# Performance work log

Measured on AMD Instinct MI355X. Metric: run time of the kernel, lower is better.

The kernel has to match this reference:

```python
import jax, jax.numpy as jnp
import numpy as np

B, S, L, D = 16, 24, 128, 768
A, T = 8, 8
VOCAB = 100


def setup_inputs() -> dict:
    key = jax.random.key(0)
    k1, k2, k3, k4, k5 = jax.random.split(key, 5)
    return {
        "sentence_embeddings": jax.random.normal(k1, (B, S, L, D), dtype=jnp.float32),
        "sentence_attention_masks": jnp.ones((B, S, L), dtype=jnp.int32),
        "sentence_ids": jax.random.randint(k2, (B, S, L), 0, VOCAB, dtype=jnp.int32),
        "predicate_ids": jax.random.randint(k3, (B, S, A, T), 0, VOCAB, dtype=jnp.int32),
        "arg0_ids": jax.random.randint(k4, (B, S, A, T), 0, VOCAB, dtype=jnp.int32),
        "arg1_ids": jax.random.randint(k5, (B, S, A, T), 0, VOCAB, dtype=jnp.int32),
    }


def _mean_pool(emb, masks):
    # emb: [B,S,L,D], masks: [B,S,L] -> [B,S,D]
    m = masks.astype(emb.dtype)
    summed = jnp.einsum("bsld,bsl->bsd", emb, m)
    counts = jnp.clip(jnp.sum(m, axis=-1, keepdims=True), 1, None)
    return summed / counts


def _arg_embedding(arg_ids, sentence_ids, emb):
    # arg_ids: [B,S,A,T] int, sentence_ids: [B,S,L] int, emb: [B,S,L,D]
    # For each arg token (id != 0), mean-pool sentence positions with matching id.
    # Original loop overwrites per token, so the result is from the LAST nonzero
    # token that has at least one match; zeros if none.
    match = (sentence_ids[:, :, None, None, :] == arg_ids[..., None]) & (
        arg_ids[..., None] != 0
    )  # [B,S,A,T,L]
    m = match.astype(emb.dtype)
    cnt = jnp.sum(m, axis=-1)  # [B,S,A,T]
    avg = jnp.einsum("bsatl,bsld->bsatd", m, emb) / jnp.maximum(cnt, 1.0)[..., None]
    valid = cnt > 0  # nonzero token AND has matches
    t_idx = jnp.arange(arg_ids.shape[-1])
    last = jnp.max(jnp.where(valid, t_idx, -1), axis=-1)  # [B,S,A]
    has_any = last >= 0
    gat = jnp.take_along_axis(
        avg, jnp.maximum(last, 0)[..., None, None], axis=3
    ).squeeze(3)  # [B,S,A,D]
    return jnp.where(has_any[..., None], gat, jnp.zeros((), emb.dtype))


def reference(sentence_embeddings, sentence_attention_masks, sentence_ids,
              predicate_ids, arg0_ids, arg1_ids):
    sentence_embeddings_avg = _mean_pool(sentence_embeddings, sentence_attention_masks)
    predicate_embeddings = _arg_embedding(predicate_ids, sentence_ids, sentence_embeddings)
    arg0_embeddings = _arg_embedding(arg0_ids, sentence_ids, sentence_embeddings)
    arg1_embeddings = _arg_embedding(arg1_ids, sentence_ids, sentence_embeddings)
    return (sentence_embeddings_avg, predicate_embeddings, arg0_embeddings, arg1_embeddings)
```

## Files before the change

### kernel.cpp

```cpp
#include <hip/hip_runtime.h>
#include <cstdint>
#include <cstddef>

#define B_ 16
#define S_ 24
#define L_ 128
#define D_ 768
#define A_ 8
#define T_ 8
#define NSLOT 24
#define HALF_D 384
#define THREADS 192
#define CHUNK 8

__global__ void __launch_bounds__(THREADS)
srl_kernel(const float* __restrict__ emb,
           const int* __restrict__ masks,
           const int* __restrict__ sids,
           const int* __restrict__ pred,
           const int* __restrict__ arg0,
           const int* __restrict__ arg1,
           float* __restrict__ out)
{
    const int blk  = blockIdx.x;
    const int bs   = blk >> 1;
    const int half = blk & 1;
    const int tid  = threadIdx.x;

    __shared__ int          sid_sh[L_];
    __shared__ float        mval_sh[L_];
    __shared__ float        inv_mask_cnt;
    __shared__ int          id_st[NSLOT][T_];
    __shared__ int          cnt_st[NSLOT][T_];
    __shared__ int          chosen_id[NSLOT];
    __shared__ float        inv_cnt[NSLOT];
    __shared__ unsigned int lmask[L_];
    __shared__ float        slot_acc[NSLOT][HALF_D];

    if (tid < L_) {
        sid_sh[tid]  = sids[bs * L_ + tid];
        mval_sh[tid] = (float)masks[bs * L_ + tid];
    }
    __syncthreads();

    {
        const int s24 = tid >> 3;
        const int t   = tid & 7;
        const int g   = s24 >> 3;
        const int a   = s24 & 7;
        const int* argp = (g == 0) ? pred : (g == 1) ? arg0 : arg1;
        const int id = argp[((bs * A_) + a) * T_ + t];
        int cnt = 0;
        if (id != 0) {
            #pragma unroll 8
            for (int l = 0; l < L_; ++l) cnt += (sid_sh[l] == id) ? 1 : 0;
        }
        id_st[s24][t]  = id;
        cnt_st[s24][t] = cnt;
    }

    {
        float* p = &slot_acc[0][0];
        for (int i = tid; i < NSLOT * HALF_D; i += THREADS) p[i] = 0.0f;
    }
    if (tid == 0) {
        float c = 0.0f;
        for (int l = 0; l < L_; ++l) c += mval_sh[l];
        inv_mask_cnt = 1.0f / fmaxf(c, 1.0f);
    }
    __syncthreads();

    if (tid < NSLOT) {
        int cid = -1;
        int ccnt = 0;
        for (int t = T_ - 1; t >= 0; --t) {
            if (cnt_st[tid][t] > 0) { cid = id_st[tid][t]; ccnt = cnt_st[tid][t]; break; }
        }
        chosen_id[tid] = cid;
        inv_cnt[tid]   = (ccnt > 0) ? (1.0f / (float)ccnt) : 0.0f;
    }
    __syncthreads();

    if (tid < L_) {
        const int s = sid_sh[tid];
        unsigned int m = 0;
        #pragma unroll
        for (int k = 0; k < NSLOT; ++k)
            m |= (unsigned int)(chosen_id[k] == s) << k;
        lmask[tid] = m;
    }
    __syncthreads();

    const int d0 = half * HALF_D + 2 * tid;
    const float* rp = emb + (size_t)bs * (L_ * D_) + d0;
    float p0 = 0.0f, p1 = 0.0f;
    for (int l0 = 0; l0 < L_; l0 += CHUNK) {
        float2 v[CHUNK];
        #pragma unroll
        for (int j = 0; j < CHUNK; ++j)
            v[j] = *(const float2*)(rp + (size_t)(l0 + j) * D_);
        #pragma unroll
        for (int j = 0; j < CHUNK; ++j) {
            const int l = l0 + j;
            const float mk = mval_sh[l];
            p0 = fmaf(v[j].x, mk, p0);
            p1 = fmaf(v[j].y, mk, p1);
            unsigned int m = lmask[l];
            while (m) {
                const int s24 = __ffs(m) - 1;
                m &= m - 1;
                float* ap = &slot_acc[s24][2 * tid];
                ap[0] += v[j].x;
                ap[1] += v[j].y;
            }
        }
    }

    {
        float2 o;
        o.x = p0 * inv_mask_cnt;
        o.y = p1 * inv_mask_cnt;
        *(float2*)(out + (size_t)bs * D_ + d0) = o;
    }
    const size_t out0_sz = (size_t)B_ * S_ * D_;
    const size_t arg_sz  = (size_t)B_ * S_ * A_ * D_;
    #pragma unroll
    for (int s24 = 0; s24 < NSLOT; ++s24) {
        const int g = s24 >> 3;
        const int a = s24 & 7;
        const float ic = inv_cnt[s24];
        const float* ap = &slot_acc[s24][2 * tid];
        float2 o;
        o.x = ap[0] * ic;
        o.y = ap[1] * ic;
        float* dst = out + out0_sz + (size_t)g * arg_sz
                   + ((size_t)(bs * A_ + a)) * D_ + d0;
        *(float2*)dst = o;
    }
}

extern "C" void kernel_launch(void* const* d_in, const int* in_sizes, int n_in,
                              void* d_out, int out_size, void* d_ws, size_t ws_size,
                              hipStream_t stream) {
    const float* emb = (const float*)d_in[0];
    const int* masks = (const int*)d_in[1];
    const int* sids  = (const int*)d_in[2];
    const int* pred  = (const int*)d_in[3];
    const int* a0    = (const int*)d_in[4];
    const int* a1    = (const int*)d_in[5];
    float* out = (float*)d_out;

    srl_kernel<<<dim3(2 * B_ * S_), dim3(THREADS), 0, stream>>>(
        emb, masks, sids, pred, a0, a1, out);
}
```

Measured before the change: 234.8 us.

## Split sequence rows across thread halves with float4 loads and shared atomics

Each block's threads now form two groups that handle even and odd sequence positions. Each thread loads float4 instead of float2, so it issues half as many row iterations and keeps more bytes in flight per load. Because both groups can add into the same argument slot, the slot accumulation now uses shared-memory atomicAdd, and the two mean-pool partial sums are combined through a small shared buffer after a barrier. The intent is better latency hiding on the streaming embedding reads, at the cost of LDS atomics and an extra reduction step.

```diff
diff --git a/kernel.cpp b/kernel.cpp
--- a/kernel.cpp
+++ b/kernel.cpp
@@ -11,6 +11,7 @@
 #define NSLOT 24
 #define HALF_D 384
 #define THREADS 192
+#define QC 96
 #define CHUNK 8
 
 __global__ void __launch_bounds__(THREADS)
@@ -26,6 +27,8 @@
     const int bs   = blk >> 1;
     const int half = blk & 1;
     const int tid  = threadIdx.x;
+    const int r    = tid / QC;
+    const int c    = tid % QC;
 
     __shared__ int          sid_sh[L_];
     __shared__ float        mval_sh[L_];
@@ -36,6 +39,7 @@
     __shared__ float        inv_cnt[NSLOT];
     __shared__ unsigned int lmask[L_];
     __shared__ float        slot_acc[NSLOT][HALF_D];
+    __shared__ float        pool_sh[QC][4];
 
     if (tid < L_) {
         sid_sh[tid]  = sids[bs * L_ + tid];
@@ -64,9 +68,9 @@
         for (int i = tid; i < NSLOT * HALF_D; i += THREADS) p[i] = 0.0f;
     }
     if (tid == 0) {
-        float c = 0.0f;
-        for (int l = 0; l < L_; ++l) c += mval_sh[l];
-        inv_mask_cnt = 1.0f / fmaxf(c, 1.0f);
+        float cm = 0.0f;
+        for (int l = 0; l < L_; ++l) cm += mval_sh[l];
+        inv_mask_cnt = 1.0f / fmaxf(cm, 1.0f);
     }
     __syncthreads();
 
@@ -91,51 +95,66 @@
     }
     __syncthreads();
 
-    const int d0 = half * HALF_D + 2 * tid;
-    const float* rp = emb + (size_t)bs * (L_ * D_) + d0;
-    float p0 = 0.0f, p1 = 0.0f;
-    for (int l0 = 0; l0 < L_; l0 += CHUNK) {
-        float2 v[CHUNK];
+    const float* rp = emb + (size_t)bs * (L_ * D_) + (size_t)r * D_
+                    + half * HALF_D + 4 * c;
+    float4 p4 = make_float4(0.f, 0.f, 0.f, 0.f);
+    for (int i0 = 0; i0 < L_ / 2; i0 += CHUNK) {
+        float4 v[CHUNK];
         #pragma unroll
         for (int j = 0; j < CHUNK; ++j)
-            v[j] = *(const float2*)(rp + (size_t)(l0 + j) * D_);
+            v[j] = *(const float4*)(rp + (size_t)(i0 + j) * (2 * D_));
         #pragma unroll
         for (int j = 0; j < CHUNK; ++j) {
-            const int l = l0 + j;
+            const int l = r + 2 * (i0 + j);
             const float mk = mval_sh[l];
-            p0 = fmaf(v[j].x, mk, p0);
-            p1 = fmaf(v[j].y, mk, p1);
+            p4.x = fmaf(v[j].x, mk, p4.x);
+            p4.y = fmaf(v[j].y, mk, p4.y);
+            p4.z = fmaf(v[j].z, mk, p4.z);
+            p4.w = fmaf(v[j].w, mk, p4.w);
             unsigned int m = lmask[l];
             while (m) {
                 const int s24 = __ffs(m) - 1;
                 m &= m - 1;
-                float* ap = &slot_acc[s24][2 * tid];
-                ap[0] += v[j].x;
-                ap[1] += v[j].y;
+                float* ap = &slot_acc[s24][4 * c];
+                atomicAdd(ap + 0, v[j].x);
+                atomicAdd(ap + 1, v[j].y);
+                atomicAdd(ap + 2, v[j].z);
+                atomicAdd(ap + 3, v[j].w);
             }
         }
     }
 
-    {
-        float2 o;
-        o.x = p0 * inv_mask_cnt;
-        o.y = p1 * inv_mask_cnt;
-        *(float2*)(out + (size_t)bs * D_ + d0) = o;
+    if (r == 1) {
+        pool_sh[c][0] = p4.x; pool_sh[c][1] = p4.y;
+        pool_sh[c][2] = p4.z; pool_sh[c][3] = p4.w;
     }
+    __syncthreads();
+
     const size_t out0_sz = (size_t)B_ * S_ * D_;
     const size_t arg_sz  = (size_t)B_ * S_ * A_ * D_;
+    const int d0 = half * HALF_D + 4 * c;
+
+    if (r == 0) {
+        float4 o;
+        o.x = (p4.x + pool_sh[c][0]) * inv_mask_cnt;
+        o.y = (p4.y + pool_sh[c][1]) * inv_mask_cnt;
+        o.z = (p4.z + pool_sh[c][2]) * inv_mask_cnt;
+        o.w = (p4.w + pool_sh[c][3]) * inv_mask_cnt;
+        *(float4*)(out + (size_t)bs * D_ + d0) = o;
+    }
     #pragma unroll
-    for (int s24 = 0; s24 < NSLOT; ++s24) {
+    for (int si = 0; si < NSLOT / 2; ++si) {
+        const int s24 = r * (NSLOT / 2) + si;
         const int g = s24 >> 3;
         const int a = s24 & 7;
         const float ic = inv_cnt[s24];
-        const float* ap = &slot_acc[s24][2 * tid];
-        float2 o;
-        o.x = ap[0] * ic;
-        o.y = ap[1] * ic;
+        const float* ap = &slot_acc[s24][4 * c];
+        float4 o;
+        o.x = ap[0] * ic; o.y = ap[1] * ic;
+        o.z = ap[2] * ic; o.w = ap[3] * ic;
         float* dst = out + out0_sz + (size_t)g * arg_sz
                    + ((size_t)(bs * A_ + a)) * D_ + d0;
-        *(float2*)dst = o;
+        *(float4*)dst = o;
     }
 }
 
```

Measured after the change: 273.4 us. 1.16x slower.
